# Kernel tuning notes

Hardware: AMD Instinct MI355X
Metric: run time of the kernel (lower is better)

## Reference

```python
import jax, jax.numpy as jnp
import numpy as np

B, T, H, Z0, D, MH = 1024, 256, 128, 64, 8, 256  # batch, time_steps, hidden, init_noise, data, mlp width


def _p(k, shape):
    s = 1.0 / np.sqrt(shape[0])
    return jax.random.uniform(k, shape, jnp.float32, -s, s)


def setup_inputs() -> dict:
    key = jax.random.key(0)
    ks = jax.random.split(key, 14)
    return {
        "init_noise": jax.random.normal(ks[0], (B, Z0), jnp.float32),
        "ts": jnp.arange(T, dtype=jnp.float32),
        "bm": jax.random.normal(ks[1], (T - 1, B, H), jnp.float32),  # standard normal; scaled by sqrt(dt)
        # initial embedding MLP: init_noise -> hidden state x0
        "iW1": _p(ks[2], (Z0, MH)), "ib1": jnp.zeros((MH,), jnp.float32),
        "iW2": _p(ks[3], (MH, H)), "ib2": jnp.zeros((H,), jnp.float32),
        # drift MLP (time dependent: input H+1)
        "fW1": _p(ks[4], (H + 1, MH)), "fb1": jnp.zeros((MH,), jnp.float32),
        "fW2": _p(ks[5], (MH, MH)), "fb2": jnp.zeros((MH,), jnp.float32),
        "fW3": _p(ks[6], (MH, H)), "fb3": jnp.zeros((H,), jnp.float32),
        # diffusion MLP (diagonal noise: output H)
        "gW1": _p(ks[7], (H + 1, MH)), "gb1": jnp.zeros((MH,), jnp.float32),
        "gW2": _p(ks[8], (MH, MH)), "gb2": jnp.zeros((MH,), jnp.float32),
        "gW3": _p(ks[9], (MH, H)), "gb3": jnp.zeros((H,), jnp.float32),
        # readout MLP: hidden -> data
        "rW1": _p(ks[10], (H, MH)), "rb1": jnp.zeros((MH,), jnp.float32),
        "rW2": _p(ks[11], (MH, D)), "rb2": jnp.zeros((D,), jnp.float32),
    }


def _mlp2(x, W1, b1, W2, b2):
    return jnp.tanh(x @ W1 + b1) @ W2 + b2


def _mlp3(x, W1, b1, W2, b2, W3, b3):
    h = jnp.tanh(x @ W1 + b1)
    h = jnp.tanh(h @ W2 + b2)
    return h @ W3 + b3


def reference(init_noise, ts, bm, iW1, ib1, iW2, ib2, fW1, fb1, fW2, fb2, fW3, fb3,
              gW1, gb1, gW2, gb2, gW3, gb3, rW1, rb1, rW2, rb2):
    dt = ts[1] - ts[0]
    sqdt = jnp.sqrt(dt)

    def f_and_g(t, x):
        # tx = cat([t, x], dim=1); time-dependent drift and diffusion
        tx = jnp.concatenate([jnp.full((x.shape[0], 1), t, x.dtype), x], axis=1)
        f = _mlp3(tx, fW1, fb1, fW2, fb2, fW3, fb3)
        g = _mlp3(tx, gW1, gb1, gW2, gb2, gW3, gb3)
        return f, g

    x0 = _mlp2(init_noise, iW1, ib1, iW2, ib2)  # [B, H]
    f0, g0 = f_and_g(ts[0], x0)

    def step(carry, inp):
        # reversible Heun (Stratonovich), as in torchsde 'reversible_heun'
        t1, z = inp
        y0, yh0, fp, gp = carry
        dW = z * sqdt  # Brownian increment ~ N(0, dt)
        yh1 = 2.0 * y0 - yh0 + fp * dt + gp * dW
        f1, g1 = f_and_g(t1, yh1)
        y1 = y0 + 0.5 * dt * (fp + f1) + 0.5 * (gp + g1) * dW
        return (y1, yh1, f1, g1), y1

    _, xs_rest = jax.lax.scan(step, (x0, x0, f0, g0), (ts[1:], bm))
    xs = jnp.concatenate([x0[None], xs_rest], axis=0).transpose(1, 0, 2)  # [B, T, H]
    ys = _mlp2(xs, rW1, rb1, rW2, rb2)  # [B, T, D]
    return ys
```

## Files before the change

kernel.cpp:

```cpp
#include <hip/hip_runtime.h>
#include <hip/hip_bf16.h>
#include <math.h>

#define NB  1024
#define T   256
#define H   128
#define Z0  64
#define D   8
#define MH  256

typedef __attribute__((ext_vector_type(8))) _Float16 half8;
typedef __attribute__((ext_vector_type(4))) _Float16 half4;
typedef __attribute__((ext_vector_type(4))) float f32x4;
typedef unsigned long long u64;

#define INV2048 4.8828125e-4f

#define OFF_F1 0
#define OFF_F2 64
#define OFF_F3 192
#define OFF_G1 256
#define OFF_G2 320
#define OFF_G3 448
#define OFF_R1 512
#define OFF_R2 576
#define OFF_I2 584
#define NFRAG  648

#define WS_HI16 0
#define WS_LO16 663552
#define WS_LO8  1327104
#define WS_EX   1658880
#define WS_FLG  4018176

#define KEEP(x) asm volatile("" : "+v"(x))

__device__ __forceinline__ f32x4 mfmaH(half8 a, half8 b, f32x4 c){
    return __builtin_amdgcn_mfma_f32_16x16x32_f16(a, b, c, 0, 0, 0);
}
__device__ __forceinline__ float ftanh(float x){
    float e = __expf(2.0f * x);
    return 1.0f - 2.0f * __builtin_amdgcn_rcpf(e + 1.0f);
}
__device__ __forceinline__ unsigned char f16_to_e5m2(_Float16 h){
    unsigned short hu = *reinterpret_cast<unsigned short*>(&h);
    return (unsigned char)((hu + 0x80) >> 8);
}
__device__ __forceinline__ half8 expandQ(u64 qw){
    unsigned int lo = (unsigned int)qw, hi = (unsigned int)(qw >> 32);
    union { unsigned int u[4]; half8 h; } u;
    u.u[0] = ((lo & 0xFFu) << 8) | ((lo & 0xFF00u) << 16);
    u.u[1] = ((lo >> 8) & 0xFF00u) | (lo & 0xFF000000u);
    u.u[2] = ((hi & 0xFFu) << 8) | ((hi & 0xFF00u) << 16);
    u.u[3] = ((hi >> 8) & 0xFF00u) | (hi & 0xFF000000u);
    return u.h;
}

__device__ __forceinline__ void st_sys4(float* p, f32x4 v){
    union { f32x4 v; u64 q[2]; } c; c.v = v;
    u64* d = reinterpret_cast<u64*>(p);
    __hip_atomic_store(d,     c.q[0], __ATOMIC_RELAXED, __HIP_MEMORY_SCOPE_SYSTEM);
    __hip_atomic_store(d + 1, c.q[1], __ATOMIC_RELAXED, __HIP_MEMORY_SCOPE_SYSTEM);
}
__device__ __forceinline__ f32x4 ld_sys4(float* p){
    union { u64 q[2]; f32x4 v; } c;
    u64* s = reinterpret_cast<u64*>(p);
    c.q[0] = __hip_atomic_load(s,     __ATOMIC_RELAXED, __HIP_MEMORY_SCOPE_SYSTEM);
    c.q[1] = __hip_atomic_load(s + 1, __ATOMIC_RELAXED, __HIP_MEMORY_SCOPE_SYSTEM);
    return c.v;
}
__device__ __forceinline__ void flag_release_sys(int* p, int v){
    __hip_atomic_store(p, v, __ATOMIC_RELAXED, __HIP_MEMORY_SCOPE_SYSTEM);
}
__device__ __forceinline__ void flag_poll_sys(int* p, int v){
    while (__hip_atomic_load(p, __ATOMIC_RELAXED, __HIP_MEMORY_SCOPE_SYSTEM) < v)
        __builtin_amdgcn_s_sleep(1);
}

__device__ __forceinline__ half8 ldB(const _Float16* buf, int sb, int kt, int b, int q){
    const char* p = reinterpret_cast<const char*>(buf);
    return *reinterpret_cast<const half8*>(p + ((b*sb + kt*64 + q*16) ^ ((b & 7) << 4)));
}
__device__ __forceinline__ void stChunk(_Float16* buf, int sb, int b, int k0, half4 v){
    char* p = reinterpret_cast<char*>(buf);
    *reinterpret_cast<half4*>(p + ((b*sb + k0*2) ^ ((b & 7) << 4))) = v;
}
__device__ __forceinline__ void stOne(_Float16* buf, int sb, int b, int k, _Float16 v){
    char* p = reinterpret_cast<char*>(buf);
    *reinterpret_cast<_Float16*>(p + ((b*sb + k*2) ^ ((b & 7) << 4))) = v;
}
__device__ __forceinline__ u64 ldsQ(const char* base, int fragRel, int l){
    return *reinterpret_cast<const u64*>(base + fragRel*512 + l*8);
}

template<bool DOTANH>
__device__ __forceinline__ void storeOut(f32x4 m, f32x4 c, _Float16* Oh, _Float16* Ol, int b, int k0){
    half4 hh, ll;
    #pragma unroll
    for (int r = 0; r < 4; ++r){
        float v = m[r] + c[r]*INV2048;
        if (DOTANH) v = ftanh(v);
        _Float16 h = (_Float16)v;
        hh[r] = h;
        ll[r] = (_Float16)((v - (float)h)*2048.0f);
    }
    stChunk(Oh, 512, b, k0, hh);
    stChunk(Ol, 512, b, k0, ll);
}
__device__ __forceinline__ void storeA1(const float* v4, _Float16* Oh, _Float16* Ol, int b, int k0){
    half4 hh, ll;
    #pragma unroll
    for (int r = 0; r < 4; ++r){
        float v = v4[r];
        _Float16 h = (_Float16)v;
        hh[r] = h;
        ll[r] = (_Float16)((v - (float)h)*2048.0f);
    }
    stChunk(Oh, 256, b, k0, hh);
    stChunk(Ol, 256, b, k0, ll);
}
__device__ __forceinline__ void stOne2(_Float16* Oh, _Float16* Ol, int b, int k, float v){
    _Float16 h = (_Float16)v;
    stOne(Oh, 512, b, k, h);
    stOne(Ol, 512, b, k, (_Float16)((v - (float)h)*2048.0f));
}

template<int KT, bool DOTANH>
__device__ __forceinline__ void layerPairReg(
    const half8* Wh0, const half8* Wh1, const half8* Wl0, const half8* Wl1,
    const _Float16* Bh, const _Float16* Bl, int sbIn,
    _Float16* Oh, _Float16* Ol, const float* bias, int n0, int n1, int b, int q)
{
    f32x4 m0 = *reinterpret_cast<const f32x4*>(bias + n0*16 + 4*q);
    f32x4 m1 = *reinterpret_cast<const f32x4*>(bias + n1*16 + 4*q);
    f32x4 c0 = {0.f,0.f,0.f,0.f}, c1 = {0.f,0.f,0.f,0.f};
    #pragma unroll
    for (int kt = 0; kt < KT; ++kt){
        half8 bh = ldB(Bh, sbIn, kt, b, q);
        half8 bl = ldB(Bl, sbIn, kt, b, q);
        m0 = mfmaH(Wh0[kt], bh, m0);
        m1 = mfmaH(Wh1[kt], bh, m1);
        c0 = mfmaH(Wh0[kt], bl, c0);
        c1 = mfmaH(Wh1[kt], bl, c1);
        c0 = mfmaH(Wl0[kt], bh, c0);
        c1 = mfmaH(Wl1[kt], bh, c1);
    }
    storeOut<DOTANH>(m0, c0, Oh, Ol, b, n0*16 + 4*q);
    storeOut<DOTANH>(m1, c1, Oh, Ol, b, n1*16 + 4*q);
}
template<int KT, bool DOTANH>
__device__ __forceinline__ void layerPairLds(
    const half8* Wh0, const half8* Wh1, const char* WloLds, int f0, int f1, int l,
    const _Float16* Bh, const _Float16* Bl, int sbIn,
    _Float16* Oh, _Float16* Ol, const float* bias, int n0, int n1, int b, int q)
{
    f32x4 m0 = *reinterpret_cast<const f32x4*>(bias + n0*16 + 4*q);
    f32x4 m1 = *reinterpret_cast<const f32x4*>(bias + n1*16 + 4*q);
    f32x4 c0 = {0.f,0.f,0.f,0.f}, c1 = {0.f,0.f,0.f,0.f};
    #pragma unroll
    for (int kt = 0; kt < KT; ++kt){
        half8 bh = ldB(Bh, sbIn, kt, b, q);
        half8 bl = ldB(Bl, sbIn, kt, b, q);
        half8 w0l = expandQ(ldsQ(WloLds, f0 + kt, l));
        half8 w1l = expandQ(ldsQ(WloLds, f1 + kt, l));
        m0 = mfmaH(Wh0[kt], bh, m0);
        m1 = mfmaH(Wh1[kt], bh, m1);
        c0 = mfmaH(Wh0[kt], bl, c0);
        c1 = mfmaH(Wh1[kt], bl, c1);
        c0 = mfmaH(w0l, bh, c0);
        c1 = mfmaH(w1l, bh, c1);
    }
    storeOut<DOTANH>(m0, c0, Oh, Ol, b, n0*16 + 4*q);
    storeOut<DOTANH>(m1, c1, Oh, Ol, b, n1*16 + 4*q);
}
__device__ __forceinline__ f32x4 layerOneLds8(
    const half8* Wh, const char* WloLds, int f0, int l,
    const _Float16* Bh, const _Float16* Bl,
    const float* bias, int n0, int b, int q)
{
    f32x4 m = *reinterpret_cast<const f32x4*>(bias + n0*16 + 4*q);
    f32x4 c = {0.f,0.f,0.f,0.f};
    #pragma unroll
    for (int kt = 0; kt < 8; ++kt){
        half8 bh = ldB(Bh, 512, kt, b, q);
        half8 bl = ldB(Bl, 512, kt, b, q);
        half8 wl = expandQ(ldsQ(WloLds, f0 + kt, l));
        m = mfmaH(Wh[kt], bh, m);
        c = mfmaH(Wh[kt], bl, c);
        c = mfmaH(wl, bh, c);
    }
    #pragma unroll
    for (int r = 0; r < 4; ++r) m[r] += c[r]*INV2048;
    return m;
}

__global__ __launch_bounds__(64)
void pack_weights(const float* __restrict__ fW1, const float* __restrict__ fW2, const float* __restrict__ fW3,
                  const float* __restrict__ gW1, const float* __restrict__ gW2, const float* __restrict__ gW3,
                  const float* __restrict__ rW1, const float* __restrict__ rW2, const float* __restrict__ iW2,
                  unsigned char* __restrict__ ws)
{
    int f = blockIdx.x, l = threadIdx.x;
    if (f >= OFF_R2 && f < OFF_I2){
        int w8r = f - OFF_R2, d = l & 15, qq = l >> 4;
        half8 v0, v1;
        #pragma unroll
        for (int j = 0; j < 8; ++j){
            int kk = qq*8 + j;
            bool ok = (d < 8) && (kk < 16);
            v0[j] = ok ? (_Float16)rW2[(w8r*16 + kk)*8 + d]        : (_Float16)0.f;
            v1[j] = ok ? (_Float16)rW2[(128 + w8r*16 + kk)*8 + d]  : (_Float16)0.f;
        }
        reinterpret_cast<half8*>(ws + WS_HI16)[(size_t)f*64 + l] = v0;
        reinterpret_cast<half8*>(ws + WS_LO16)[(size_t)f*64 + l] = v1;
        *reinterpret_cast<u64*>(ws + WS_LO8 + (size_t)f*512 + l*8) = 0ull;
        return;
    }
    const float* W; int KT, base, ld, ncols;
    if      (f <  64) { W = fW1+256; KT=4; base=OFF_F1; ld=256; ncols=256; }
    else if (f < 192) { W = fW2;     KT=8; base=OFF_F2; ld=256; ncols=256; }
    else if (f < 256) { W = fW3;     KT=8; base=OFF_F3; ld=128; ncols=128; }
    else if (f < 320) { W = gW1+256; KT=4; base=OFF_G1; ld=256; ncols=256; }
    else if (f < 448) { W = gW2;     KT=8; base=OFF_G2; ld=256; ncols=256; }
    else if (f < 512) { W = gW3;     KT=8; base=OFF_G3; ld=128; ncols=128; }
    else if (f < 576) { W = rW1;     KT=4; base=OFF_R1; ld=256; ncols=256; }
    else              { W = iW2;     KT=8; base=OFF_I2; ld=128; ncols=128; }
    int rel = f - base, n = rel / KT, kt = rel % KT;
    int krow = kt*32 + (l >> 4)*8;
    int col  = n*16  + (l & 15);
    half8 vh, vl; u64 qw = 0;
    #pragma unroll
    for (int j = 0; j < 8; ++j){
        float x = (col < ncols) ? W[(size_t)(krow + j)*ld + col] : 0.0f;
        _Float16 h = (_Float16)x;
        vh[j] = h;
        _Float16 r16 = (_Float16)((x - (float)h) * 2048.0f);
        vl[j] = r16;
        qw |= (u64)f16_to_e5m2(r16) << (8*j);
    }
    reinterpret_cast<half8*>(ws + WS_HI16)[(size_t)f*64 + l] = vh;
    reinterpret_cast<half8*>(ws + WS_LO16)[(size_t)f*64 + l] = vl;
    *reinterpret_cast<u64*>(ws + WS_LO8 + (size_t)f*512 + l*8) = qw;
}

__global__ __launch_bounds__(256)
void zero_flags(unsigned char* ws){
    int* fl = (int*)(ws + WS_FLG);
    #pragma unroll
    for (int i = 0; i < 16; ++i) fl[threadIdx.x + i*256] = 0;
}

__global__ __launch_bounds__(256)
void prefill_out(const float* __restrict__ rb2, float* __restrict__ out){
    f32x4 v0, v1;
    #pragma unroll
    for (int r = 0; r < 4; ++r){ v0[r] = rb2[r]; v1[r] = rb2[4+r]; }
    size_t i = ((size_t)blockIdx.x*256 + threadIdx.x)*2;
    f32x4* o = reinterpret_cast<f32x4*>(out);
    o[i] = v0; o[i+1] = v1;
}

__global__ __launch_bounds__(512, 2)
void sde_main(const float* __restrict__ init_noise, const float* __restrict__ ts,
              const float* __restrict__ bm,
              const float* __restrict__ iW1, const float* __restrict__ ib1,
              const float* __restrict__ ib2,
              const float* __restrict__ fb1, const float* __restrict__ fW1r,
              const float* __restrict__ fb2, const float* __restrict__ fb3,
              const float* __restrict__ gb1, const float* __restrict__ gW1r,
              const float* __restrict__ gb2, const float* __restrict__ gb3,
              const float* __restrict__ rb1,
              unsigned char* __restrict__ ws,
              float* __restrict__ out)
{
    const int tid  = threadIdx.x;
    const int wv   = tid >> 6;
    const int l    = tid & 63;
    const int q    = l >> 4;
    const int b    = l & 15;
    const int bid  = blockIdx.x;
    const int role  = (bid >= 64) ? 1 : 0;
    const int group = bid & 63;
    const int row0  = group * 16;
    const int w8    = wv;

    __shared__ __align__(16) char Wlo2[65536];
    __shared__ __align__(16) char Wlo3[32768];
    __shared__ __align__(16) _Float16 A1h[16*128], A1l[16*128];
    __shared__ __align__(16) _Float16 H1h[16*256], H1l[16*256];
    __shared__ __align__(16) _Float16 H2h[16*256], H2l[16*256];
    __shared__ __align__(16) _Float16 Y1[16*128];
    __shared__ __align__(16) _Float16 Rb[8*256];
    __shared__ __align__(16) float s_b1[256];
    __shared__ __align__(16) float s_w1r0[256];
    __shared__ __align__(16) float s_bp[256];
    __shared__ __align__(16) float s_b2[256];
    __shared__ __align__(16) float s_b3[128];
    __shared__ __align__(16) float s_rb1h[128];

    const float* b1p = role ? gb1 : fb1;
    const float* w1p = role ? gW1r : fW1r;
    const float* b2p = role ? gb2 : fb2;
    const float* b3p = role ? gb3 : fb3;
    const int o1 = role ? OFF_G1 : OFF_F1;
    const int o2 = role ? OFF_G2 : OFF_F2;
    const int o3 = role ? OFF_G3 : OFF_F3;

    char* exg = (char*)ws + WS_EX + (size_t)group*36864;
    float* Xown = (float*)(exg + role*18432);
    float* Xpar = (float*)(exg + (1-role)*18432);
    int* flags   = (int*)(ws + WS_FLG + (size_t)group*256);
    int* flagOwn = flags + role;
    int* flagPar = flags + (1 - role);

    if (tid < 256){ s_b1[tid] = b1p[tid]; s_w1r0[tid] = w1p[tid]; s_b2[tid] = b2p[tid]; }
    else if (tid < 384){ s_b3[tid-256] = b3p[tid-256]; }
    else { s_rb1h[tid-384] = rb1[role*128 + (tid-384)]; }
    float* zb = reinterpret_cast<float*>(H2h);
    zb[tid]       = init_noise[row0*Z0 + tid];
    zb[tid + 512] = init_noise[row0*Z0 + 512 + tid];
    {
        f32x4* d2 = (f32x4*)Wlo2; const f32x4* s2 = (const f32x4*)(ws + WS_LO8 + (size_t)o2*512);
        #pragma unroll
        for (int i = 0; i < 8; ++i) d2[tid + i*512] = s2[tid + i*512];
        f32x4* d3 = (f32x4*)Wlo3; const f32x4* s3 = (const f32x4*)(ws + WS_LO8 + (size_t)o3*512);
        #pragma unroll
        for (int i = 0; i < 4; ++i) d3[tid + i*512] = s3[tid + i*512];
    }
    const half8* hi  = reinterpret_cast<const half8*>(ws + WS_HI16);
    const half8* lo16 = reinterpret_cast<const half8*>(ws + WS_LO16);
    half8 W1h[2][4], W1l[2][4], W2h[2][8], W3h[8], WR1[4], WR2;
    #pragma unroll
    for (int kt = 0; kt < 4; ++kt){
        W1h[0][kt] = hi  [(size_t)(o1 + (2*w8  )*4 + kt)*64 + l];
        W1h[1][kt] = hi  [(size_t)(o1 + (2*w8+1)*4 + kt)*64 + l];
        W1l[0][kt] = lo16[(size_t)(o1 + (2*w8  )*4 + kt)*64 + l];
        W1l[1][kt] = lo16[(size_t)(o1 + (2*w8+1)*4 + kt)*64 + l];
        WR1[kt]    = hi  [(size_t)(OFF_R1 + (role*8 + w8)*4 + kt)*64 + l];
    }
    #pragma unroll
    for (int kt = 0; kt < 8; ++kt){
        W2h[0][kt] = hi[(size_t)(o2 + (2*w8  )*8 + kt)*64 + l];
        W2h[1][kt] = hi[(size_t)(o2 + (2*w8+1)*8 + kt)*64 + l];
        W3h[kt]    = hi[(size_t)(o3 + w8*8 + kt)*64 + l];
    }
    WR2 = role ? lo16[(size_t)(OFF_R2 + w8)*64 + l] : hi[(size_t)(OFF_R2 + w8)*64 + l];

    #pragma unroll
    for (int s = 0; s < 2; ++s){
        #pragma unroll
        for (int kt = 0; kt < 4; ++kt){ KEEP(W1h[s][kt]); KEEP(W1l[s][kt]); }
        #pragma unroll
        for (int kt = 0; kt < 8; ++kt){ KEEP(W2h[s][kt]); }
    }
    #pragma unroll
    for (int kt = 0; kt < 8; ++kt){ KEEP(W3h[kt]); }
    __syncthreads();

    {
        const int c = tid & 255, hf = tid >> 8;
        float ac[8]; float bv = ib1[c];
        #pragma unroll
        for (int rr = 0; rr < 8; ++rr) ac[rr] = bv;
        for (int k = 0; k < Z0; ++k){
            float wt = iW1[k*256 + c];
            #pragma unroll
            for (int rr = 0; rr < 8; ++rr) ac[rr] += zb[(hf*8+rr)*Z0 + k] * wt;
        }
        #pragma unroll
        for (int rr = 0; rr < 8; ++rr) stOne2(H1h, H1l, hf*8+rr, c, ftanh(ac[rr]));
    }
    __syncthreads();

    float y[4], yh[4], fp[4], gp[4], bmv[4];
    {
        half8 ih[8], il[8];
        #pragma unroll
        for (int kt = 0; kt < 8; ++kt){
            ih[kt] = hi  [(size_t)(OFF_I2 + w8*8 + kt)*64 + l];
            il[kt] = lo16[(size_t)(OFF_I2 + w8*8 + kt)*64 + l];
        }
        f32x4 m = *reinterpret_cast<const f32x4*>(ib2 + w8*16 + 4*q);
        f32x4 c = {0.f,0.f,0.f,0.f};
        #pragma unroll
        for (int kt = 0; kt < 8; ++kt){
            half8 bh = ldB(H1h, 512, kt, b, q);
            half8 bl = ldB(H1l, 512, kt, b, q);
            m = mfmaH(ih[kt], bh, m);
            c = mfmaH(ih[kt], bl, c);
            c = mfmaH(il[kt], bh, c);
        }
        float xv[4]; half4 hv;
        #pragma unroll
        for (int r = 0; r < 4; ++r){
            float v = m[r] + c[r]*INV2048;
            y[r] = v; yh[r] = v; xv[r] = v; bmv[r] = 0.f;
            hv[r] = (_Float16)v;
        }
        storeA1(xv, A1h, A1l, b, w8*16 + 4*q);
        stChunk(Y1, 256, b, w8*16 + 4*q, hv);
    }

    const float ts0  = ts[0];
    const float dtv  = ts[1] - ts0;
    const float sqdt = sqrtf(dtv);

    #pragma unroll 1
    for (int t = 0; t < T; ++t){
        const float tval = ts0 + (float)t * dtv;
        const int par = t & 1;
        float dWv[4] = {0.f,0.f,0.f,0.f};
        if (t > 0){
            float nv[4];
            #pragma unroll
            for (int r = 0; r < 4; ++r){
                dWv[r] = bmv[r] * sqdt;
                float nyh = 2.0f*y[r] - yh[r] + fp[r]*dtv + gp[r]*dWv[r];
                yh[r] = nyh; nv[r] = nyh;
            }
            storeA1(nv, A1h, A1l, b, w8*16 + 4*q);
        }
        if (tid < 256) s_bp[tid] = s_b1[tid] + tval * s_w1r0[tid];
        __syncthreads();
        if (t < T-1){
            f32x4 bv = *reinterpret_cast<const f32x4*>(
                bm + (size_t)t*(NB*H) + (size_t)(row0+b)*H + w8*16 + 4*q);
            #pragma unroll
            for (int r = 0; r < 4; ++r) bmv[r] = bv[r];
        }
        layerPairReg<4, true>(W1h[0], W1h[1], W1l[0], W1l[1],
                              A1h, A1l, 256, H1h, H1l, s_bp, 2*w8, 2*w8+1, b, q);
        __syncthreads();
        layerPairLds<8, true>(W2h[0], W2h[1], Wlo2, (2*w8)*8, (2*w8+1)*8, l,
                              H1h, H1l, 512, H2h, H2l, s_b2, 2*w8, 2*w8+1, b, q);
        __syncthreads();
        f32x4 v3 = layerOneLds8(W3h, Wlo3, w8*8, l, H2h, H2l, s_b3, w8, b, q);
        st_sys4(Xown + par*2304 + (b*128 + w8*16 + 4*q), v3);
        f32x4 pr = {0.f,0.f,0.f,0.f};
        if (t > 0){
            f32x4 m = *reinterpret_cast<const f32x4*>(s_rb1h + w8*16 + 4*q);
            #pragma unroll
            for (int kt = 0; kt < 4; ++kt) m = mfmaH(WR1[kt], ldB(Y1, 256, kt, b, q), m);
            half4 hv;
            #pragma unroll
            for (int r = 0; r < 4; ++r) hv[r] = (_Float16)ftanh(m[r]);
            *reinterpret_cast<half4*>(&Rb[w8*256 + b*16 + 4*q]) = hv;
            half8 bf = *reinterpret_cast<const half8*>(&Rb[w8*256 + b*16 + (q&1)*8]);
            pr = mfmaH(WR2, bf, pr);
        }
        __syncthreads();
        if (tid == 0) flag_release_sys(flagOwn, t + 1);
        if (t > 0 && q < 2){
            float* op = out + (size_t)(row0+b)*(T*D) + (size_t)(t-1)*D + 4*q;
            #pragma unroll
            for (int r = 0; r < 4; ++r) atomicAdd(op + r, pr[r]);
        }
        if (tid == 0) flag_poll_sys(flagPar, t + 1);
        __syncthreads();
        f32x4 vp = ld_sys4(Xpar + par*2304 + (b*128 + w8*16 + 4*q));
        {
            half4 hv;
            #pragma unroll
            for (int r = 0; r < 4; ++r){
                float fn = role ? vp[r] : v3[r];
                float gn = role ? v3[r] : vp[r];
                if (t > 0) y[r] += 0.5f*dtv*(fp[r] + fn) + 0.5f*(gp[r] + gn)*dWv[r];
                fp[r] = fn; gp[r] = gn;
                hv[r] = (_Float16)y[r];
            }
            stChunk(Y1, 256, b, w8*16 + 4*q, hv);
        }
    }

    __syncthreads();
    {
        f32x4 m = *reinterpret_cast<const f32x4*>(s_rb1h + w8*16 + 4*q);
        #pragma unroll
        for (int kt = 0; kt < 4; ++kt) m = mfmaH(WR1[kt], ldB(Y1, 256, kt, b, q), m);
        half4 hv;
        #pragma unroll
        for (int r = 0; r < 4; ++r) hv[r] = (_Float16)ftanh(m[r]);
        *reinterpret_cast<half4*>(&Rb[w8*256 + b*16 + 4*q]) = hv;
        half8 bf = *reinterpret_cast<const half8*>(&Rb[w8*256 + b*16 + (q&1)*8]);
        f32x4 pr = {0.f,0.f,0.f,0.f};
        pr = mfmaH(WR2, bf, pr);
        if (q < 2){
            float* op = out + (size_t)(row0+b)*(T*D) + (size_t)(T-1)*D + 4*q;
            #pragma unroll
            for (int r = 0; r < 4; ++r) atomicAdd(op + r, pr[r]);
        }
    }
}

extern "C" void kernel_launch(void* const* d_in, const int* in_sizes, int n_in,
                              void* d_out, int out_size, void* d_ws, size_t ws_size,
                              hipStream_t stream)
{
    const float* init_noise = (const float*)d_in[0];
    const float* ts  = (const float*)d_in[1];
    const float* bm  = (const float*)d_in[2];
    const float* iW1 = (const float*)d_in[3];
    const float* ib1 = (const float*)d_in[4];
    const float* iW2 = (const float*)d_in[5];
    const float* ib2 = (const float*)d_in[6];
    const float* fW1 = (const float*)d_in[7];
    const float* fb1 = (const float*)d_in[8];
    const float* fW2 = (const float*)d_in[9];
    const float* fb2 = (const float*)d_in[10];
    const float* fW3 = (const float*)d_in[11];
    const float* fb3 = (const float*)d_in[12];
    const float* gW1 = (const float*)d_in[13];
    const float* gb1 = (const float*)d_in[14];
    const float* gW2 = (const float*)d_in[15];
    const float* gb2 = (const float*)d_in[16];
    const float* gW3 = (const float*)d_in[17];
    const float* gb3 = (const float*)d_in[18];
    const float* rW1 = (const float*)d_in[19];
    const float* rb1 = (const float*)d_in[20];
    const float* rW2 = (const float*)d_in[21];
    const float* rb2 = (const float*)d_in[22];

    unsigned char* ws = (unsigned char*)d_ws;

    zero_flags<<<dim3(1), dim3(256), 0, stream>>>(ws);
    pack_weights<<<dim3(NFRAG), dim3(64), 0, stream>>>(
        fW1, fW2, fW3, gW1, gW2, gW3, rW1, rW2, iW2, ws);
    prefill_out<<<dim3(1024), dim3(256), 0, stream>>>(rb2, (float*)d_out);
    sde_main<<<dim3(128), dim3(512), 0, stream>>>(
        init_noise, ts, bm, iW1, ib1, ib2,
        fb1, fW1, fb2, fb3,
        gb1, gW1, gb2, gb3,
        rb1, ws, (float*)d_out);
}
```

Baseline: 2.073 ms.

## Probe partner coherence at agent scope and use cheaper barriers in step loop

Before the loop, thread 0 of each block runs a ping-pong handshake with its partner block using agent-scope atomics under a timeout. If both sides pass, the time loop switches its exchange stores, loads and flag polling from system scope to agent scope, which is meant to cut cross-XCD synchronisation latency. It also replaces several __syncthreads with raw s_barrier (with or without an lgkmcnt wait) to avoid extra waits. The risk is that agent-scope visibility across dies may be unsafe in cases the probe does not catch, and that a raw barrier without a full wait could expose a race.

```diff
diff --git a/kernel.cpp b/kernel.cpp
--- a/kernel.cpp
+++ b/kernel.cpp
@@ -35,6 +35,9 @@
 
 #define KEEP(x) asm volatile("" : "+v"(x))
 
+#define BAR_LGKM() asm volatile("s_waitcnt lgkmcnt(0)\n\ts_barrier" ::: "memory")
+#define BAR_ONLY() asm volatile("s_barrier" ::: "memory")
+
 __device__ __forceinline__ f32x4 mfmaH(half8 a, half8 b, f32x4 c){
     return __builtin_amdgcn_mfma_f32_16x16x32_f16(a, b, c, 0, 0, 0);
 }
@@ -69,12 +72,30 @@
     c.q[1] = __hip_atomic_load(s + 1, __ATOMIC_RELAXED, __HIP_MEMORY_SCOPE_SYSTEM);
     return c.v;
 }
-__device__ __forceinline__ void flag_release_sys(int* p, int v){
+__device__ __forceinline__ void st_sys_i(int* p, int v){
     __hip_atomic_store(p, v, __ATOMIC_RELAXED, __HIP_MEMORY_SCOPE_SYSTEM);
 }
-__device__ __forceinline__ void flag_poll_sys(int* p, int v){
-    while (__hip_atomic_load(p, __ATOMIC_RELAXED, __HIP_MEMORY_SCOPE_SYSTEM) < v)
-        __builtin_amdgcn_s_sleep(1);
+__device__ __forceinline__ int ld_sys_i(int* p){
+    return __hip_atomic_load(p, __ATOMIC_RELAXED, __HIP_MEMORY_SCOPE_SYSTEM);
+}
+__device__ __forceinline__ void st_ag4(float* p, f32x4 v){
+    union { f32x4 v; u64 q[2]; } c; c.v = v;
+    u64* d = reinterpret_cast<u64*>(p);
+    __hip_atomic_store(d,     c.q[0], __ATOMIC_RELAXED, __HIP_MEMORY_SCOPE_AGENT);
+    __hip_atomic_store(d + 1, c.q[1], __ATOMIC_RELAXED, __HIP_MEMORY_SCOPE_AGENT);
+}
+__device__ __forceinline__ f32x4 ld_ag4(float* p){
+    union { u64 q[2]; f32x4 v; } c;
+    u64* s = reinterpret_cast<u64*>(p);
+    c.q[0] = __hip_atomic_load(s,     __ATOMIC_RELAXED, __HIP_MEMORY_SCOPE_AGENT);
+    c.q[1] = __hip_atomic_load(s + 1, __ATOMIC_RELAXED, __HIP_MEMORY_SCOPE_AGENT);
+    return c.v;
+}
+__device__ __forceinline__ void st_ag_i(int* p, int v){
+    __hip_atomic_store(p, v, __ATOMIC_RELAXED, __HIP_MEMORY_SCOPE_AGENT);
+}
+__device__ __forceinline__ int ld_ag_i(int* p){
+    return __hip_atomic_load(p, __ATOMIC_RELAXED, __HIP_MEMORY_SCOPE_AGENT);
 }
 
 __device__ __forceinline__ half8 ldB(const _Float16* buf, int sb, int kt, int b, int q){
@@ -297,6 +318,7 @@
     __shared__ __align__(16) float s_b2[256];
     __shared__ __align__(16) float s_b3[128];
     __shared__ __align__(16) float s_rb1h[128];
+    __shared__ int s_fast;
 
     const float* b1p = role ? gb1 : fb1;
     const float* w1p = role ? gW1r : fW1r;
@@ -312,6 +334,10 @@
     int* flags   = (int*)(ws + WS_FLG + (size_t)group*256);
     int* flagOwn = flags + role;
     int* flagPar = flags + (1 - role);
+    int* tokOwn  = flags + 2 + role;
+    int* tokPar  = flags + 2 + (1 - role);
+    int* decOwn  = flags + 4 + role;
+    int* decPar  = flags + 4 + (1 - role);
 
     if (tid < 256){ s_b1[tid] = b1p[tid]; s_w1r0[tid] = w1p[tid]; s_b2[tid] = b2p[tid]; }
     else if (tid < 384){ s_b3[tid-256] = b3p[tid-256]; }
@@ -355,7 +381,26 @@
     }
     #pragma unroll
     for (int kt = 0; kt < 8; ++kt){ KEEP(W3h[kt]); }
+
+    if (tid == 0){
+        int okv = 1;
+        for (int i = 1; i <= 24; ++i){
+            st_ag_i(tokOwn, i);
+            u64 dl = (i == 1) ? 60000ull : 1600ull;
+            u64 st = __builtin_amdgcn_s_memrealtime();
+            while (ld_ag_i(tokPar) < i){
+                if (__builtin_amdgcn_s_memrealtime() - st > dl){ okv = 0; break; }
+                __builtin_amdgcn_s_sleep(1);
+            }
+            if (!okv) break;
+        }
+        st_sys_i(decOwn, okv + 1);
+        int pd;
+        while ((pd = ld_sys_i(decPar)) == 0) __builtin_amdgcn_s_sleep(1);
+        s_fast = (okv == 1 && pd == 2) ? 1 : 0;
+    }
     __syncthreads();
+    const int fastp = s_fast;
 
     {
         const int c = tid & 255, hf = tid >> 8;
@@ -421,7 +466,7 @@
             storeA1(nv, A1h, A1l, b, w8*16 + 4*q);
         }
         if (tid < 256) s_bp[tid] = s_b1[tid] + tval * s_w1r0[tid];
-        __syncthreads();
+        BAR_LGKM();
         if (t < T-1){
             f32x4 bv = *reinterpret_cast<const f32x4*>(
                 bm + (size_t)t*(NB*H) + (size_t)(row0+b)*H + w8*16 + 4*q);
@@ -430,12 +475,13 @@
         }
         layerPairReg<4, true>(W1h[0], W1h[1], W1l[0], W1l[1],
                               A1h, A1l, 256, H1h, H1l, s_bp, 2*w8, 2*w8+1, b, q);
-        __syncthreads();
+        BAR_LGKM();
         layerPairLds<8, true>(W2h[0], W2h[1], Wlo2, (2*w8)*8, (2*w8+1)*8, l,
                               H1h, H1l, 512, H2h, H2l, s_b2, 2*w8, 2*w8+1, b, q);
-        __syncthreads();
+        BAR_LGKM();
         f32x4 v3 = layerOneLds8(W3h, Wlo3, w8*8, l, H2h, H2l, s_b3, w8, b, q);
-        st_sys4(Xown + par*2304 + (b*128 + w8*16 + 4*q), v3);
+        if (fastp) st_ag4(Xown + par*2304 + (b*128 + w8*16 + 4*q), v3);
+        else       st_sys4(Xown + par*2304 + (b*128 + w8*16 + 4*q), v3);
         f32x4 pr = {0.f,0.f,0.f,0.f};
         if (t > 0){
             f32x4 m = *reinterpret_cast<const f32x4*>(s_rb1h + w8*16 + 4*q);
@@ -449,15 +495,22 @@
             pr = mfmaH(WR2, bf, pr);
         }
         __syncthreads();
-        if (tid == 0) flag_release_sys(flagOwn, t + 1);
+        if (tid == 0){
+            if (fastp) st_ag_i(flagOwn, t + 1);
+            else       st_sys_i(flagOwn, t + 1);
+        }
         if (t > 0 && q < 2){
             float* op = out + (size_t)(row0+b)*(T*D) + (size_t)(t-1)*D + 4*q;
             #pragma unroll
             for (int r = 0; r < 4; ++r) atomicAdd(op + r, pr[r]);
         }
-        if (tid == 0) flag_poll_sys(flagPar, t + 1);
-        __syncthreads();
-        f32x4 vp = ld_sys4(Xpar + par*2304 + (b*128 + w8*16 + 4*q));
+        if (tid == 0){
+            if (fastp){ while (ld_ag_i(flagPar) < t + 1) __builtin_amdgcn_s_sleep(1); }
+            else      { while (ld_sys_i(flagPar) < t + 1) __builtin_amdgcn_s_sleep(1); }
+        }
+        BAR_ONLY();
+        f32x4 vp = fastp ? ld_ag4(Xpar + par*2304 + (b*128 + w8*16 + 4*q))
+                         : ld_sys4(Xpar + par*2304 + (b*128 + w8*16 + 4*q));
         {
             half4 hv;
             #pragma unroll
```

After: 2.174 ms. 1.05x slower.

## Double block to 1024 threads, one output tile per wave, split readout waves

Applied to the files above, without the earlier changes.

Each block of the persistent SDE kernel now runs 16 waves instead of 8. Every wave computes a single 16-column tile of layers 1 and 2 rather than a pair. The final layer and state update stay on the first 8 waves, and the readout MLP moves onto the other 8, so it can run alongside layer 3. The intent is more latency hiding and fewer serialized MFMA chains per wave on the critical recurrent path, at the cost of more block-wide barriers and more register pressure under launch bounds of 1024.

```diff
diff --git a/kernel.cpp b/kernel.cpp
--- a/kernel.cpp
+++ b/kernel.cpp
@@ -69,12 +69,11 @@
     c.q[1] = __hip_atomic_load(s + 1, __ATOMIC_RELAXED, __HIP_MEMORY_SCOPE_SYSTEM);
     return c.v;
 }
-__device__ __forceinline__ void flag_release_sys(int* p, int v){
+__device__ __forceinline__ void st_sys_i(int* p, int v){
     __hip_atomic_store(p, v, __ATOMIC_RELAXED, __HIP_MEMORY_SCOPE_SYSTEM);
 }
-__device__ __forceinline__ void flag_poll_sys(int* p, int v){
-    while (__hip_atomic_load(p, __ATOMIC_RELAXED, __HIP_MEMORY_SCOPE_SYSTEM) < v)
-        __builtin_amdgcn_s_sleep(1);
+__device__ __forceinline__ int ld_sys_i(int* p){
+    return __hip_atomic_load(p, __ATOMIC_RELAXED, __HIP_MEMORY_SCOPE_SYSTEM);
 }
 
 __device__ __forceinline__ half8 ldB(const _Float16* buf, int sb, int kt, int b, int q){
@@ -125,53 +124,40 @@
     stOne(Ol, 512, b, k, (_Float16)((v - (float)h)*2048.0f));
 }
 
-template<int KT, bool DOTANH>
-__device__ __forceinline__ void layerPairReg(
-    const half8* Wh0, const half8* Wh1, const half8* Wl0, const half8* Wl1,
+__device__ __forceinline__ void layerOneReg4(
+    const half8* Wh, const half8* Wl,
     const _Float16* Bh, const _Float16* Bl, int sbIn,
-    _Float16* Oh, _Float16* Ol, const float* bias, int n0, int n1, int b, int q)
+    _Float16* Oh, _Float16* Ol, const float* bias, int n, int b, int q)
 {
-    f32x4 m0 = *reinterpret_cast<const f32x4*>(bias + n0*16 + 4*q);
-    f32x4 m1 = *reinterpret_cast<const f32x4*>(bias + n1*16 + 4*q);
-    f32x4 c0 = {0.f,0.f,0.f,0.f}, c1 = {0.f,0.f,0.f,0.f};
-    #pragma unroll
-    for (int kt = 0; kt < KT; ++kt){
+    f32x4 m = *reinterpret_cast<const f32x4*>(bias + n*16 + 4*q);
+    f32x4 c = {0.f,0.f,0.f,0.f};
+    #pragma unroll
+    for (int kt = 0; kt < 4; ++kt){
         half8 bh = ldB(Bh, sbIn, kt, b, q);
         half8 bl = ldB(Bl, sbIn, kt, b, q);
-        m0 = mfmaH(Wh0[kt], bh, m0);
-        m1 = mfmaH(Wh1[kt], bh, m1);
-        c0 = mfmaH(Wh0[kt], bl, c0);
-        c1 = mfmaH(Wh1[kt], bl, c1);
-        c0 = mfmaH(Wl0[kt], bh, c0);
-        c1 = mfmaH(Wl1[kt], bh, c1);
-    }
-    storeOut<DOTANH>(m0, c0, Oh, Ol, b, n0*16 + 4*q);
-    storeOut<DOTANH>(m1, c1, Oh, Ol, b, n1*16 + 4*q);
-}
-template<int KT, bool DOTANH>
-__device__ __forceinline__ void layerPairLds(
-    const half8* Wh0, const half8* Wh1, const char* WloLds, int f0, int f1, int l,
-    const _Float16* Bh, const _Float16* Bl, int sbIn,
-    _Float16* Oh, _Float16* Ol, const float* bias, int n0, int n1, int b, int q)
+        m = mfmaH(Wh[kt], bh, m);
+        c = mfmaH(Wh[kt], bl, c);
+        c = mfmaH(Wl[kt], bh, c);
+    }
+    storeOut<true>(m, c, Oh, Ol, b, n*16 + 4*q);
+}
+__device__ __forceinline__ void layerOneLds2(
+    const half8* Wh, const char* WloLds, int f0, int l,
+    const _Float16* Bh, const _Float16* Bl,
+    _Float16* Oh, _Float16* Ol, const float* bias, int n, int b, int q)
 {
-    f32x4 m0 = *reinterpret_cast<const f32x4*>(bias + n0*16 + 4*q);
-    f32x4 m1 = *reinterpret_cast<const f32x4*>(bias + n1*16 + 4*q);
-    f32x4 c0 = {0.f,0.f,0.f,0.f}, c1 = {0.f,0.f,0.f,0.f};
-    #pragma unroll
-    for (int kt = 0; kt < KT; ++kt){
-        half8 bh = ldB(Bh, sbIn, kt, b, q);
-        half8 bl = ldB(Bl, sbIn, kt, b, q);
-        half8 w0l = expandQ(ldsQ(WloLds, f0 + kt, l));
-        half8 w1l = expandQ(ldsQ(WloLds, f1 + kt, l));
-        m0 = mfmaH(Wh0[kt], bh, m0);
-        m1 = mfmaH(Wh1[kt], bh, m1);
-        c0 = mfmaH(Wh0[kt], bl, c0);
-        c1 = mfmaH(Wh1[kt], bl, c1);
-        c0 = mfmaH(w0l, bh, c0);
-        c1 = mfmaH(w1l, bh, c1);
-    }
-    storeOut<DOTANH>(m0, c0, Oh, Ol, b, n0*16 + 4*q);
-    storeOut<DOTANH>(m1, c1, Oh, Ol, b, n1*16 + 4*q);
+    f32x4 m = *reinterpret_cast<const f32x4*>(bias + n*16 + 4*q);
+    f32x4 c = {0.f,0.f,0.f,0.f};
+    #pragma unroll
+    for (int kt = 0; kt < 8; ++kt){
+        half8 bh = ldB(Bh, 512, kt, b, q);
+        half8 bl = ldB(Bl, 512, kt, b, q);
+        half8 wl = expandQ(ldsQ(WloLds, f0 + kt, l));
+        m = mfmaH(Wh[kt], bh, m);
+        c = mfmaH(Wh[kt], bl, c);
+        c = mfmaH(wl, bh, c);
+    }
+    storeOut<true>(m, c, Oh, Ol, b, n*16 + 4*q);
 }
 __device__ __forceinline__ f32x4 layerOneLds8(
     const half8* Wh, const char* WloLds, int f0, int l,
@@ -260,7 +246,7 @@
     o[i] = v0; o[i+1] = v1;
 }
 
-__global__ __launch_bounds__(512, 2)
+__global__ __launch_bounds__(1024, 4)
 void sde_main(const float* __restrict__ init_noise, const float* __restrict__ ts,
               const float* __restrict__ bm,
               const float* __restrict__ iW1, const float* __restrict__ ib1,
@@ -274,7 +260,7 @@
               float* __restrict__ out)
 {
     const int tid  = threadIdx.x;
-    const int wv   = tid >> 6;
+    const int w16  = tid >> 6;
     const int l    = tid & 63;
     const int q    = l >> 4;
     const int b    = l & 15;
@@ -282,7 +268,8 @@
     const int role  = (bid >= 64) ? 1 : 0;
     const int group = bid & 63;
     const int row0  = group * 16;
-    const int w8    = wv;
+    const bool stateW = (w16 < 8);
+    const int wr   = w16 - 8;
 
     __shared__ __align__(16) char Wlo2[65536];
     __shared__ __align__(16) char Wlo3[32768];
@@ -315,72 +302,68 @@
 
     if (tid < 256){ s_b1[tid] = b1p[tid]; s_w1r0[tid] = w1p[tid]; s_b2[tid] = b2p[tid]; }
     else if (tid < 384){ s_b3[tid-256] = b3p[tid-256]; }
-    else { s_rb1h[tid-384] = rb1[role*128 + (tid-384)]; }
+    else if (tid < 512){ s_rb1h[tid-384] = rb1[role*128 + (tid-384)]; }
     float* zb = reinterpret_cast<float*>(H2h);
-    zb[tid]       = init_noise[row0*Z0 + tid];
-    zb[tid + 512] = init_noise[row0*Z0 + 512 + tid];
+    zb[tid] = init_noise[row0*Z0 + tid];
     {
         f32x4* d2 = (f32x4*)Wlo2; const f32x4* s2 = (const f32x4*)(ws + WS_LO8 + (size_t)o2*512);
         #pragma unroll
-        for (int i = 0; i < 8; ++i) d2[tid + i*512] = s2[tid + i*512];
+        for (int i = 0; i < 4; ++i) d2[tid + i*1024] = s2[tid + i*1024];
         f32x4* d3 = (f32x4*)Wlo3; const f32x4* s3 = (const f32x4*)(ws + WS_LO8 + (size_t)o3*512);
         #pragma unroll
-        for (int i = 0; i < 4; ++i) d3[tid + i*512] = s3[tid + i*512];
+        for (int i = 0; i < 2; ++i) d3[tid + i*1024] = s3[tid + i*1024];
     }
     const half8* hi  = reinterpret_cast<const half8*>(ws + WS_HI16);
     const half8* lo16 = reinterpret_cast<const half8*>(ws + WS_LO16);
-    half8 W1h[2][4], W1l[2][4], W2h[2][8], W3h[8], WR1[4], WR2;
+    half8 W1h[4], W1l[4], W2h[8], WX[8];
     #pragma unroll
     for (int kt = 0; kt < 4; ++kt){
-        W1h[0][kt] = hi  [(size_t)(o1 + (2*w8  )*4 + kt)*64 + l];
-        W1h[1][kt] = hi  [(size_t)(o1 + (2*w8+1)*4 + kt)*64 + l];
-        W1l[0][kt] = lo16[(size_t)(o1 + (2*w8  )*4 + kt)*64 + l];
-        W1l[1][kt] = lo16[(size_t)(o1 + (2*w8+1)*4 + kt)*64 + l];
-        WR1[kt]    = hi  [(size_t)(OFF_R1 + (role*8 + w8)*4 + kt)*64 + l];
+        W1h[kt] = hi  [(size_t)(o1 + w16*4 + kt)*64 + l];
+        W1l[kt] = lo16[(size_t)(o1 + w16*4 + kt)*64 + l];
     }
     #pragma unroll
     for (int kt = 0; kt < 8; ++kt){
-        W2h[0][kt] = hi[(size_t)(o2 + (2*w8  )*8 + kt)*64 + l];
-        W2h[1][kt] = hi[(size_t)(o2 + (2*w8+1)*8 + kt)*64 + l];
-        W3h[kt]    = hi[(size_t)(o3 + w8*8 + kt)*64 + l];
-    }
-    WR2 = role ? lo16[(size_t)(OFF_R2 + w8)*64 + l] : hi[(size_t)(OFF_R2 + w8)*64 + l];
-
-    #pragma unroll
-    for (int s = 0; s < 2; ++s){
-        #pragma unroll
-        for (int kt = 0; kt < 4; ++kt){ KEEP(W1h[s][kt]); KEEP(W1l[s][kt]); }
-        #pragma unroll
-        for (int kt = 0; kt < 8; ++kt){ KEEP(W2h[s][kt]); }
-    }
-    #pragma unroll
-    for (int kt = 0; kt < 8; ++kt){ KEEP(W3h[kt]); }
+        W2h[kt] = hi[(size_t)(o2 + w16*8 + kt)*64 + l];
+    }
+    if (stateW){
+        #pragma unroll
+        for (int kt = 0; kt < 8; ++kt) WX[kt] = hi[(size_t)(o3 + w16*8 + kt)*64 + l];
+    } else {
+        #pragma unroll
+        for (int kt = 0; kt < 4; ++kt) WX[kt] = hi[(size_t)(OFF_R1 + (role*8 + wr)*4 + kt)*64 + l];
+        WX[4] = role ? lo16[(size_t)(OFF_R2 + wr)*64 + l] : hi[(size_t)(OFF_R2 + wr)*64 + l];
+        WX[5] = WX[4]; WX[6] = WX[4]; WX[7] = WX[4];
+    }
+    #pragma unroll
+    for (int kt = 0; kt < 4; ++kt){ KEEP(W1h[kt]); KEEP(W1l[kt]); }
+    #pragma unroll
+    for (int kt = 0; kt < 8; ++kt){ KEEP(W2h[kt]); KEEP(WX[kt]); }
     __syncthreads();
 
     {
         const int c = tid & 255, hf = tid >> 8;
-        float ac[8]; float bv = ib1[c];
-        #pragma unroll
-        for (int rr = 0; rr < 8; ++rr) ac[rr] = bv;
+        float ac[4]; float bv = ib1[c];
+        #pragma unroll
+        for (int rr = 0; rr < 4; ++rr) ac[rr] = bv;
         for (int k = 0; k < Z0; ++k){
             float wt = iW1[k*256 + c];
             #pragma unroll
-            for (int rr = 0; rr < 8; ++rr) ac[rr] += zb[(hf*8+rr)*Z0 + k] * wt;
-        }
-        #pragma unroll
-        for (int rr = 0; rr < 8; ++rr) stOne2(H1h, H1l, hf*8+rr, c, ftanh(ac[rr]));
+            for (int rr = 0; rr < 4; ++rr) ac[rr] += zb[(hf*4+rr)*Z0 + k] * wt;
+        }
+        #pragma unroll
+        for (int rr = 0; rr < 4; ++rr) stOne2(H1h, H1l, hf*4+rr, c, ftanh(ac[rr]));
     }
     __syncthreads();
 
     float y[4], yh[4], fp[4], gp[4], bmv[4];
-    {
+    if (stateW){
         half8 ih[8], il[8];
         #pragma unroll
         for (int kt = 0; kt < 8; ++kt){
-            ih[kt] = hi  [(size_t)(OFF_I2 + w8*8 + kt)*64 + l];
-            il[kt] = lo16[(size_t)(OFF_I2 + w8*8 + kt)*64 + l];
-        }
-        f32x4 m = *reinterpret_cast<const f32x4*>(ib2 + w8*16 + 4*q);
+            ih[kt] = hi  [(size_t)(OFF_I2 + w16*8 + kt)*64 + l];
+            il[kt] = lo16[(size_t)(OFF_I2 + w16*8 + kt)*64 + l];
+        }
+        f32x4 m = *reinterpret_cast<const f32x4*>(ib2 + w16*16 + 4*q);
         f32x4 c = {0.f,0.f,0.f,0.f};
         #pragma unroll
         for (int kt = 0; kt < 8; ++kt){
@@ -397,8 +380,8 @@
             y[r] = v; yh[r] = v; xv[r] = v; bmv[r] = 0.f;
             hv[r] = (_Float16)v;
         }
-        storeA1(xv, A1h, A1l, b, w8*16 + 4*q);
-        stChunk(Y1, 256, b, w8*16 + 4*q, hv);
+        storeA1(xv, A1h, A1l, b, w16*16 + 4*q);
+        stChunk(Y1, 256, b, w16*16 + 4*q, hv);
     }
 
     const float ts0  = ts[0];
@@ -410,7 +393,7 @@
         const float tval = ts0 + (float)t * dtv;
         const int par = t & 1;
         float dWv[4] = {0.f,0.f,0.f,0.f};
-        if (t > 0){
+        if (stateW && t > 0){
             float nv[4];
             #pragma unroll
             for (int r = 0; r < 4; ++r){
@@ -418,47 +401,52 @@
                 float nyh = 2.0f*y[r] - yh[r] + fp[r]*dtv + gp[r]*dWv[r];
                 yh[r] = nyh; nv[r] = nyh;
             }
-            storeA1(nv, A1h, A1l, b, w8*16 + 4*q);
-        }
-        if (tid < 256) s_bp[tid] = s_b1[tid] + tval * s_w1r0[tid];
+            storeA1(nv, A1h, A1l, b, w16*16 + 4*q);
+        }
+        if (tid >= 512 && tid < 768){
+            int c = tid - 512;
+            s_bp[c] = s_b1[c] + tval * s_w1r0[c];
+        }
         __syncthreads();
-        if (t < T-1){
+        if (stateW && t < T-1){
             f32x4 bv = *reinterpret_cast<const f32x4*>(
-                bm + (size_t)t*(NB*H) + (size_t)(row0+b)*H + w8*16 + 4*q);
+                bm + (size_t)t*(NB*H) + (size_t)(row0+b)*H + w16*16 + 4*q);
             #pragma unroll
             for (int r = 0; r < 4; ++r) bmv[r] = bv[r];
         }
-        layerPairReg<4, true>(W1h[0], W1h[1], W1l[0], W1l[1],
-                              A1h, A1l, 256, H1h, H1l, s_bp, 2*w8, 2*w8+1, b, q);
+        layerOneReg4(W1h, W1l, A1h, A1l, 256, H1h, H1l, s_bp, w16, b, q);
         __syncthreads();
-        layerPairLds<8, true>(W2h[0], W2h[1], Wlo2, (2*w8)*8, (2*w8+1)*8, l,
-                              H1h, H1l, 512, H2h, H2l, s_b2, 2*w8, 2*w8+1, b, q);
+        layerOneLds2(W2h, Wlo2, w16*8, l, H1h, H1l, H2h, H2l, s_b2, w16, b, q);
         __syncthreads();
-        f32x4 v3 = layerOneLds8(W3h, Wlo3, w8*8, l, H2h, H2l, s_b3, w8, b, q);
-        st_sys4(Xown + par*2304 + (b*128 + w8*16 + 4*q), v3);
+        f32x4 v3 = {0.f,0.f,0.f,0.f};
         f32x4 pr = {0.f,0.f,0.f,0.f};
-        if (t > 0){
-            f32x4 m = *reinterpret_cast<const f32x4*>(s_rb1h + w8*16 + 4*q);
-            #pragma unroll
-            for (int kt = 0; kt < 4; ++kt) m = mfmaH(WR1[kt], ldB(Y1, 256, kt, b, q), m);
+        if (stateW){
+            v3 = layerOneLds8(WX, Wlo3, w16*8, l, H2h, H2l, s_b3, w16, b, q);
+            st_sys4(Xown + par*2304 + (b*128 + w16*16 + 4*q), v3);
+        } else if (t > 0){
+            f32x4 m = *reinterpret_cast<const f32x4*>(s_rb1h + wr*16 + 4*q);
+            #pragma unroll
+            for (int kt = 0; kt < 4; ++kt) m = mfmaH(WX[kt], ldB(Y1, 256, kt, b, q), m);
             half4 hv;
             #pragma unroll
             for (int r = 0; r < 4; ++r) hv[r] = (_Float16)ftanh(m[r]);
-            *reinterpret_cast<half4*>(&Rb[w8*256 + b*16 + 4*q]) = hv;
-            half8 bf = *reinterpret_cast<const half8*>(&Rb[w8*256 + b*16 + (q&1)*8]);
-            pr = mfmaH(WR2, bf, pr);
+            *reinterpret_cast<half4*>(&Rb[wr*256 + b*16 + 4*q]) = hv;
+            half8 bf = *reinterpret_cast<const half8*>(&Rb[wr*256 + b*16 + (q&1)*8]);
+            pr = mfmaH(WX[4], bf, pr);
         }
         __syncthreads();
-        if (tid == 0) flag_release_sys(flagOwn, t + 1);
-        if (t > 0 && q < 2){
+        if (tid == 0) st_sys_i(flagOwn, t + 1);
+        if (!stateW && t > 0 && q < 2){
             float* op = out + (size_t)(row0+b)*(T*D) + (size_t)(t-1)*D + 4*q;
             #pragma unroll
             for (int r = 0; r < 4; ++r) atomicAdd(op + r, pr[r]);
         }
-        if (tid == 0) flag_poll_sys(flagPar, t + 1);
+        if (tid == 0){
+            while (ld_sys_i(flagPar) < t + 1) __builtin_amdgcn_s_sleep(1);
+        }
         __syncthreads();
-        f32x4 vp = ld_sys4(Xpar + par*2304 + (b*128 + w8*16 + 4*q));
-        {
+        if (stateW){
+            f32x4 vp = ld_sys4(Xpar + par*2304 + (b*128 + w16*16 + 4*q));
             half4 hv;
             #pragma unroll
             for (int r = 0; r < 4; ++r){
@@ -468,22 +456,22 @@
                 fp[r] = fn; gp[r] = gn;
                 hv[r] = (_Float16)y[r];
             }
-            stChunk(Y1, 256, b, w8*16 + 4*q, hv);
+            stChunk(Y1, 256, b, w16*16 + 4*q, hv);
         }
     }
 
     __syncthreads();
-    {
-        f32x4 m = *reinterpret_cast<const f32x4*>(s_rb1h + w8*16 + 4*q);
-        #pragma unroll
-        for (int kt = 0; kt < 4; ++kt) m = mfmaH(WR1[kt], ldB(Y1, 256, kt, b, q), m);
+    if (!stateW){
+        f32x4 m = *reinterpret_cast<const f32x4*>(s_rb1h + wr*16 + 4*q);
+        #pragma unroll
+        for (int kt = 0; kt < 4; ++kt) m = mfmaH(WX[kt], ldB(Y1, 256, kt, b, q), m);
         half4 hv;
         #pragma unroll
         for (int r = 0; r < 4; ++r) hv[r] = (_Float16)ftanh(m[r]);
-        *reinterpret_cast<half4*>(&Rb[w8*256 + b*16 + 4*q]) = hv;
-        half8 bf = *reinterpret_cast<const half8*>(&Rb[w8*256 + b*16 + (q&1)*8]);
+        *reinterpret_cast<half4*>(&Rb[wr*256 + b*16 + 4*q]) = hv;
+        half8 bf = *reinterpret_cast<const half8*>(&Rb[wr*256 + b*16 + (q&1)*8]);
         f32x4 pr = {0.f,0.f,0.f,0.f};
-        pr = mfmaH(WR2, bf, pr);
+        pr = mfmaH(WX[4], bf, pr);
         if (q < 2){
             float* op = out + (size_t)(row0+b)*(T*D) + (size_t)(T-1)*D + 4*q;
             #pragma unroll
@@ -526,7 +514,7 @@
     pack_weights<<<dim3(NFRAG), dim3(64), 0, stream>>>(
         fW1, fW2, fW3, gW1, gW2, gW3, rW1, rW2, iW2, ws);
     prefill_out<<<dim3(1024), dim3(256), 0, stream>>>(rb2, (float*)d_out);
-    sde_main<<<dim3(128), dim3(512), 0, stream>>>(
+    sde_main<<<dim3(128), dim3(1024), 0, stream>>>(
         init_noise, ts, bm, iW1, ib1, ib2,
         fb1, fW1, fb2, fb3,
         gb1, gW1, gb2, gb3,
```

New measurement: 2.821 ms. 36.1% more time.
